# Kernel tuning notes

Measured on AMD Instinct MI355X. Metric: run time of the kernel, lower is better.

Reference implementation:

```python
import jax, jax.numpy as jnp
import numpy as np

GROUPS = 32
EPS = 1e-6

def group_norm(x, gamma, beta):
    # x: [B,C,H,W]
    B, C, H, W = x.shape
    xg = x.reshape(B, GROUPS, C // GROUPS, H, W)
    mu = xg.mean(axis=(2, 3, 4), keepdims=True)
    var = xg.var(axis=(2, 3, 4), keepdims=True)
    xn = ((xg - mu) * jax.lax.rsqrt(var + EPS)).reshape(B, C, H, W)
    return xn * gamma[None, :, None, None] + beta[None, :, None, None]

def setup_inputs() -> dict:
    key = jax.random.key(0)
    ks = jax.random.split(key, 12)
    B, C, H, W = 4, 256, 64, 64
    s = 1.0 / np.sqrt(C)
    return {
        "x": jax.random.normal(ks[0], (B, C, H, W), jnp.float32),
        "gn_gamma": jnp.ones((C,), jnp.float32),
        "gn_beta": jnp.zeros((C,), jnp.float32),
        "wq": jax.random.normal(ks[1], (C, C), jnp.float32) * s,
        "bq": jnp.zeros((C,), jnp.float32),
        "wk": jax.random.normal(ks[2], (C, C), jnp.float32) * s,
        "bk": jnp.zeros((C,), jnp.float32),
        "wv": jax.random.normal(ks[3], (C, C), jnp.float32) * s,
        "bv": jnp.zeros((C,), jnp.float32),
        "wu": jax.random.normal(ks[4], (1, C), jnp.float32) * s,
        "bu": jnp.zeros((1,), jnp.float32),
        "wp": jax.random.normal(ks[5], (C, C), jnp.float32) * s,
        "bp": jnp.zeros((C,), jnp.float32),
    }

def reference(x, gn_gamma, gn_beta, wq, bq, wk, bk, wv, bv, wu, bu, wp, bp):
    B, C, H, W = x.shape
    hw = H * W
    hn = group_norm(x, gn_gamma, gn_beta)          # norm(x); context=x so same norm
    t = hn.reshape(B, C, hw).transpose(0, 2, 1)    # [B, hw, C]
    q = t @ wq.T + bq                              # 1x1 conv == per-token linear
    k = t @ wk.T + bk
    v = t @ wv.T + bv
    u_map = jax.nn.sigmoid(t @ wu.T + bu)          # [B, hw, 1]
    scale = jnp.asarray(C, x.dtype) ** -0.5
    scores = jnp.einsum('bic,bjc->bij', q, k) * scale * u_map.transpose(0, 2, 1)
    attn = jax.nn.softmax(scores, axis=2)          # softmax over keys j
    out = jnp.einsum('bij,bjc->bic', attn, v)      # [B, hw, C]
    out = (out @ wp.T + bp).transpose(0, 2, 1).reshape(B, C, H, W)
    return (x + out, u_map)
```

## Files before the change

### kernel.cpp

```cpp
#include <hip/hip_runtime.h>
#include <cstdint>

#define B_ 4
#define C_ 256
#define HW_ 4096
#define CPG_ 8
#define M_TOT 16384
#define SCALE 0.0625f
#define FLASH_LDS 133120

typedef __attribute__((ext_vector_type(4))) float f32x4;
typedef __attribute__((ext_vector_type(16))) float f32x16;
typedef __attribute__((ext_vector_type(8))) unsigned short u16x8;
typedef __attribute__((ext_vector_type(4))) unsigned short u16x4;
typedef __attribute__((ext_vector_type(4))) unsigned int u32x4;
typedef __attribute__((ext_vector_type(8))) __bf16 bf16x8;

static __device__ __forceinline__ unsigned short f2bf(float f) {
  unsigned int u = __builtin_bit_cast(unsigned int, f);
  u += 0x7fffu + ((u >> 16) & 1u);
  return (unsigned short)(u >> 16);
}
static __device__ __forceinline__ float bf2f(unsigned short s) {
  return __builtin_bit_cast(float, ((unsigned int)s) << 16);
}
static __device__ __forceinline__ bf16x8 ldbf8(const unsigned short* p) {
  return __builtin_bit_cast(bf16x8, *(const u16x8*)p);
}
static __device__ __forceinline__ bf16x8 cvt8(const float* p) {
  f32x4 a = *(const f32x4*)p;
  f32x4 b = *(const f32x4*)(p + 4);
  u16x8 r;
  r[0] = f2bf(a[0]); r[1] = f2bf(a[1]); r[2] = f2bf(a[2]); r[3] = f2bf(a[3]);
  r[4] = f2bf(b[0]); r[5] = f2bf(b[1]); r[6] = f2bf(b[2]); r[7] = f2bf(b[3]);
  return __builtin_bit_cast(bf16x8, r);
}
static __device__ __forceinline__ void gload16(const void* g, void* l) {
  __builtin_amdgcn_global_load_lds(
      (const __attribute__((address_space(1))) unsigned int*)g,
      (__attribute__((address_space(3))) unsigned int*)l, 16, 0, 0);
}
static __device__ __forceinline__ unsigned cvtpk(float lo, float hi) {
  unsigned r;
  asm("v_cvt_pk_bf16_f32 %0, %1, %2" : "=v"(r) : "v"(lo), "v"(hi));
  return r;
}

__global__ __launch_bounds__(256) void gn_kernel(const float* __restrict__ x,
    const float* __restrict__ gamma, const float* __restrict__ beta,
    unsigned short* __restrict__ t) {
  int bg = blockIdx.x;
  int b = bg >> 5, g = bg & 31;
  const float* xp = x + ((size_t)(b * C_ + g * CPG_)) * HW_;
  float s = 0.f, ss = 0.f;
  for (int i = threadIdx.x; i < CPG_ * HW_; i += 256) {
    float v = xp[i]; s += v; ss += v * v;
  }
#pragma unroll
  for (int m = 32; m; m >>= 1) { s += __shfl_xor(s, m); ss += __shfl_xor(ss, m); }
  __shared__ float red[8];
  if ((threadIdx.x & 63) == 0) { red[threadIdx.x >> 6] = s; red[4 + (threadIdx.x >> 6)] = ss; }
  __syncthreads();
  float S = red[0] + red[1] + red[2] + red[3];
  float SS = red[4] + red[5] + red[6] + red[7];
  float mean = S * (1.f / 32768.f);
  float var = SS * (1.f / 32768.f) - mean * mean;
  float rs = rsqrtf(var + 1e-6f);
  float gam[CPG_], bet[CPG_];
#pragma unroll
  for (int cc = 0; cc < CPG_; ++cc) {
    float gm = gamma[g * CPG_ + cc];
    gam[cc] = gm * rs;
    bet[cc] = beta[g * CPG_ + cc] - mean * gm * rs;
  }
  for (int sp = threadIdx.x; sp < HW_; sp += 256) {
    u16x8 o;
#pragma unroll
    for (int cc = 0; cc < CPG_; ++cc) {
      float v = xp[cc * HW_ + sp];
      o[cc] = f2bf(v * gam[cc] + bet[cc]);
    }
    *(u16x8*)(t + ((size_t)(b * HW_ + sp)) * C_ + g * CPG_) = o;
  }
}

__global__ __launch_bounds__(256) void u_kernel(const unsigned short* __restrict__ t,
    const float* __restrict__ wu, const float* __restrict__ bu,
    float* __restrict__ uout) {
  int w = threadIdx.x >> 6, l = threadIdx.x & 63;
  int tok = blockIdx.x * 4 + w;
  u16x4 tv = *(const u16x4*)(t + (size_t)tok * C_ + l * 4);
  f32x4 wv4 = *(const f32x4*)(wu + l * 4);
  float d = bf2f(tv[0]) * wv4[0] + bf2f(tv[1]) * wv4[1] +
            bf2f(tv[2]) * wv4[2] + bf2f(tv[3]) * wv4[3];
#pragma unroll
  for (int m = 32; m; m >>= 1) d += __shfl_xor(d, m);
  if (l == 0) uout[tok] = 1.f / (1.f + __expf(-(d + bu[0])));
}

__global__ __launch_bounds__(256, 2) void qkv_kernel(const unsigned short* __restrict__ t,
    const float* __restrict__ wq, const float* __restrict__ wk, const float* __restrict__ wv,
    const float* __restrict__ bq, const float* __restrict__ bk, const float* __restrict__ bv,
    const float* __restrict__ uu,
    unsigned short* __restrict__ q, unsigned short* __restrict__ k,
    unsigned short* __restrict__ vt) {
  int mblk = blockIdx.x, nblk = blockIdx.y;
  int wsel = nblk >> 2;
  int n0 = (nblk & 3) * 64;
  const float* W = wsel == 0 ? wq : (wsel == 1 ? wk : wv);
  const float* bias = wsel == 0 ? bq : (wsel == 1 ? bk : bv);
  __shared__ unsigned short WL[64][264];
  int tid = threadIdx.x;
#pragma unroll
  for (int p = 0; p < 8; ++p) {
    int row = p * 8 + (tid >> 5);
    int kc0 = (tid & 31) * 8;
    *(bf16x8*)&WL[row][kc0] = cvt8(W + (size_t)(n0 + row) * C_ + kc0);
  }
  __syncthreads();
  int wid = tid >> 6, l = tid & 63;
  int lr = l & 15, lg = l >> 4;
  int row = mblk * 64 + wid * 16 + lr;
  f32x4 acc[4] = {};
  const unsigned short* ap = t + (size_t)row * C_ + lg * 8;
#pragma unroll
  for (int kc = 0; kc < 8; ++kc) {
    bf16x8 a = ldbf8(ap + kc * 32);
#pragma unroll
    for (int j = 0; j < 4; ++j) {
      bf16x8 bb = ldbf8(&WL[j * 16 + lr][kc * 32 + lg * 8]);
      acc[j] = __builtin_amdgcn_mfma_f32_16x16x32_bf16(a, bb, acc[j], 0, 0, 0);
    }
  }
  if (wsel < 2) {
    unsigned short* dst = wsel ? k : q;
    float su[4] = {1.f, 1.f, 1.f, 1.f};
    if (wsel == 1) {
      f32x4 u4 = *(const f32x4*)(uu + mblk * 64 + wid * 16 + lg * 4);
      su[0] = SCALE * u4[0]; su[1] = SCALE * u4[1];
      su[2] = SCALE * u4[2]; su[3] = SCALE * u4[3];
    }
#pragma unroll
    for (int j = 0; j < 4; ++j) {
      int col = n0 + j * 16 + lr;
      float bv_ = bias[col];
#pragma unroll
      for (int r = 0; r < 4; ++r)
        dst[(size_t)(mblk * 64 + wid * 16 + lg * 4 + r) * C_ + col] =
            f2bf((acc[j][r] + bv_) * su[r]);
    }
  } else {
    __shared__ float lds[64][65];
#pragma unroll
    for (int j = 0; j < 4; ++j) {
      float bv_ = bias[n0 + j * 16 + lr];
#pragma unroll
      for (int r = 0; r < 4; ++r)
        lds[wid * 16 + lg * 4 + r][j * 16 + lr] = acc[j][r] + bv_;
    }
    __syncthreads();
    int bb_ = (mblk * 64) >> 12;
    int s0 = (mblk * 64) & 4095;
    int ss = tid & 63, cc0 = tid >> 6;
    for (int cc = cc0; cc < 64; cc += 4)
      vt[((size_t)(bb_ * C_ + n0 + cc)) * HW_ + s0 + ss] = f2bf(lds[ss][cc]);
  }
}

__global__ __launch_bounds__(256, 1) void flash_kernel(const unsigned short* __restrict__ q,
    const unsigned short* __restrict__ k, const unsigned short* __restrict__ vt,
    unsigned short* __restrict__ o) {
  extern __shared__ char smem[];
  float* cmb_m = (float*)(smem + 131072);
  float* cmb_l = (float*)(smem + 131584);
  float* facw  = (float*)(smem + 132096);
  float* scrL  = (float*)(smem + 132608);

  int blk = blockIdx.x;
  int b = blk >> 6;
  int qrow0 = (blk & 63) * 64;
  int tid = threadIdx.x;
  int wid = tid >> 6, l = tid & 63;
  int l5 = l & 31, hi = l >> 5;
  int h = wid >> 1, qs = wid & 1;

  const unsigned short* kb = k + (size_t)b * HW_ * C_;
  const unsigned short* vb = vt + (size_t)b * C_ * HW_;

  bf16x8 qreg[16];
  {
    const unsigned short* qp = q + ((size_t)b * HW_ + qrow0 + qs * 32 + l5) * C_ + hi * 8;
#pragma unroll
    for (int cc = 0; cc < 16; ++cc) qreg[cc] = ldbf8(qp + cc * 16);
  }

  f32x16 oa[8];
#pragma unroll
  for (int ct = 0; ct < 8; ++ct)
#pragma unroll
    for (int r = 0; r < 16; ++r) oa[ct][r] = 0.f;
  float mrow = -1e30f, lrow = 0.f;

  int w_ = l >> 2;
  int w0_ = w_ & 1, w1_ = (w_ >> 1) & 1, w2_ = (w_ >> 2) & 1, w3_ = (w_ >> 3) & 1;
  int koffb = (l & 3) * 8;

#define STAGE(IT, BUFN)                                                          \
  {                                                                              \
    int key0n = h * 2048 + (IT) * 32;                                            \
    if (qs == 0) {                                                               \
      _Pragma("unroll")                                                          \
      for (int j = 0; j < 16; ++j) {                                             \
        int key = j * 2 + hi;                                                    \
        const unsigned short* g =                                                \
            kb + (size_t)(key0n + key) * C_ + ((l5 * 8) ^ (key * 8));            \
        gload16(g, smem + (BUFN) * 32768 + h * 16384 + j * 1024);                \
      }                                                                          \
    } else {                                                                     \
      _Pragma("unroll")                                                          \
      for (int j = 0; j < 16; ++j) {                                             \
        int j0 = j & 1;                                                          \
        int ch = (j << 4) | (w3_ << 3) | ((w2_ ^ j0) << 2) |                     \
                 ((w1_ ^ w3_) << 1) | (w0_ ^ w2_ ^ j0);                          \
        int ke = koffb ^ ((ch & 3) << 3);                                        \
        const unsigned short* g = vb + (size_t)ch * HW_ + key0n + ke;            \
        gload16(g, smem + 65536 + (BUFN) * 32768 + h * 16384 + j * 1024);        \
      }                                                                          \
    }                                                                            \
  }

  STAGE(0, 0);
  __syncthreads();

  int kx = l5 << 4;
  int vbase = (l5 * 64) ^ ((l5 >> 2) << 6);
  int ko0 = (hi * 16) ^ ((l & 3) << 4);
  int ko1 = (32 + hi * 16) ^ ((l & 3) << 4);

  for (int it = 0; it < 64; ++it) {
    int buf = it & 1;
    if (it + 1 < 64) STAGE(it + 1, buf ^ 1);

    const char* KB = smem + buf * 32768 + h * 16384;
    f32x16 s;
#pragma unroll
    for (int r = 0; r < 16; ++r) s[r] = 0.f;
#pragma unroll
    for (int cc = 0; cc < 16; ++cc) {
      bf16x8 kf = ldbf8((const unsigned short*)(KB + l5 * 512 +
                                                ((cc * 32 + hi * 16) ^ kx)));
      s = __builtin_amdgcn_mfma_f32_32x32x16_bf16(kf, qreg[cc], s, 0, 0, 0);
    }

    float mxl = s[0];
#pragma unroll
    for (int r = 1; r < 16; ++r) mxl = fmaxf(mxl, s[r]);
    float mx = fmaxf(mxl, __shfl_xor(mxl, 32));
    if (!__all(mx <= mrow + 8.f)) {
      float mnew = fmaxf(mrow, mx);
      float scr = __expf(mrow - mnew);
      mrow = mnew;
      lrow *= scr;
      if (hi == 0) scrL[wid * 32 + l5] = scr;
      float sr[16];
#pragma unroll
      for (int r = 0; r < 16; ++r)
        sr[r] = scrL[wid * 32 + (r & 3) + 8 * (r >> 2) + 4 * hi];
#pragma unroll
      for (int ct = 0; ct < 8; ++ct)
#pragma unroll
        for (int r = 0; r < 16; ++r) oa[ct][r] *= sr[r];
    }
    unsigned wp[8];
#pragma unroll
    for (int rp = 0; rp < 8; ++rp) {
      float e0 = __expf(s[2 * rp] - mrow);
      float e1 = __expf(s[2 * rp + 1] - mrow);
      lrow += e0 + e1;
      wp[rp] = cvtpk(e0, e1);
    }
    unsigned sx[8];
#pragma unroll
    for (int rp = 0; rp < 8; ++rp) sx[rp] = (unsigned)__shfl_xor((int)wp[rp], 32);
    bool hib = (hi != 0);
    u32x4 pa0u = {hib ? sx[2] : wp[0], hib ? sx[3] : wp[1],
                  hib ? wp[2] : sx[0], hib ? wp[3] : sx[1]};
    u32x4 pa1u = {hib ? sx[6] : wp[4], hib ? sx[7] : wp[5],
                  hib ? wp[6] : sx[4], hib ? wp[7] : sx[5]};
    bf16x8 pa0 = __builtin_bit_cast(bf16x8, pa0u);
    bf16x8 pa1 = __builtin_bit_cast(bf16x8, pa1u);

    const char* VB = smem + 65536 + buf * 32768 + h * 16384;
#pragma unroll
    for (int ct = 0; ct < 8; ++ct) {
      bf16x8 v0 = ldbf8((const unsigned short*)(VB + ct * 2048 + vbase + ko0));
      bf16x8 v1 = ldbf8((const unsigned short*)(VB + ct * 2048 + vbase + ko1));
      oa[ct] = __builtin_amdgcn_mfma_f32_32x32x16_bf16(pa0, v0, oa[ct], 0, 0, 0);
      oa[ct] = __builtin_amdgcn_mfma_f32_32x32x16_bf16(pa1, v1, oa[ct], 0, 0, 0);
    }
    __syncthreads();
  }
#undef STAGE

  float l_all = lrow + __shfl_xor(lrow, 32);
  if (hi == 0) { cmb_m[wid * 32 + l5] = mrow; cmb_l[wid * 32 + l5] = l_all; }
  __syncthreads();
  float mo = cmb_m[(wid ^ 2) * 32 + l5];
  float lo = cmb_l[(wid ^ 2) * 32 + l5];
  float M = fmaxf(mrow, mo);
  float el = __expf(mrow - M), eo = __expf(mo - M);
  float fac = el / (l_all * el + lo * eo);
  if (hi == 0) facw[wid * 32 + l5] = fac;
  float fr[16];
#pragma unroll
  for (int r = 0; r < 16; ++r)
    fr[r] = facw[wid * 32 + (r & 3) + 8 * (r >> 2) + 4 * hi];
  float* Ow = (float*)(smem + wid * 32768);
#pragma unroll
  for (int ct = 0; ct < 8; ++ct)
#pragma unroll
    for (int r = 0; r < 16; ++r) {
      int qr = (r & 3) + 8 * (r >> 2) + 4 * hi;
      Ow[qr * 256 + ct * 32 + l5] = oa[ct][r] * fr[r];
    }
  __syncthreads();
  for (int e = tid; e < 2048; e += 256) {
    int row = e >> 5;
    int c8 = (e & 31) * 8;
    int qs_ = row >> 5, q_ = row & 31;
    const float* p0 = (const float*)(smem + qs_ * 32768) + q_ * 256 + c8;
    const float* p1 = (const float*)(smem + (2 + qs_) * 32768) + q_ * 256 + c8;
    u16x8 ov;
#pragma unroll
    for (int j = 0; j < 8; ++j) ov[j] = f2bf(p0[j] + p1[j]);
    *(u16x8*)(o + ((size_t)b * HW_ + qrow0 + row) * C_ + c8) = ov;
  }
}

__global__ __launch_bounds__(256, 2) void proj_kernel(const unsigned short* __restrict__ o,
    const float* __restrict__ wp, const float* __restrict__ bp,
    const float* __restrict__ x, float* __restrict__ y) {
  int mblk = blockIdx.x, nblk = blockIdx.y;
  int n0 = nblk * 64;
  __shared__ unsigned short WL[64][264];
  int tid = threadIdx.x;
#pragma unroll
  for (int p = 0; p < 8; ++p) {
    int row = p * 8 + (tid >> 5);
    int kc0 = (tid & 31) * 8;
    *(bf16x8*)&WL[row][kc0] = cvt8(wp + (size_t)(n0 + row) * C_ + kc0);
  }
  __syncthreads();
  int wid = tid >> 6, l = tid & 63;
  int lr = l & 15, lg = l >> 4;
  int row = mblk * 64 + wid * 16 + lr;
  f32x4 acc[4] = {};
  const unsigned short* ap = o + (size_t)row * C_ + lg * 8;
#pragma unroll
  for (int kc = 0; kc < 8; ++kc) {
    bf16x8 a = ldbf8(ap + kc * 32);
#pragma unroll
    for (int j = 0; j < 4; ++j) {
      bf16x8 bb = ldbf8(&WL[j * 16 + lr][kc * 32 + lg * 8]);
      acc[j] = __builtin_amdgcn_mfma_f32_16x16x32_bf16(a, bb, acc[j], 0, 0, 0);
    }
  }
  __shared__ float lds[64][65];
#pragma unroll
  for (int j = 0; j < 4; ++j) {
    float bv_ = bp[n0 + j * 16 + lr];
#pragma unroll
    for (int r = 0; r < 4; ++r)
      lds[wid * 16 + lg * 4 + r][j * 16 + lr] = acc[j][r] + bv_;
  }
  __syncthreads();
  int bb_ = (mblk * 64) >> 12;
  int s0 = (mblk * 64) & 4095;
  int ss = tid & 63, cc0 = tid >> 6;
  for (int cc = cc0; cc < 64; cc += 4) {
    size_t idx = ((size_t)(bb_ * C_ + n0 + cc)) * HW_ + s0 + ss;
    y[idx] = x[idx] + lds[ss][cc];
  }
}

extern "C" void kernel_launch(void* const* d_in, const int* in_sizes, int n_in,
                              void* d_out, int out_size, void* d_ws, size_t ws_size,
                              hipStream_t stream) {
  const float* x     = (const float*)d_in[0];
  const float* gamma = (const float*)d_in[1];
  const float* beta  = (const float*)d_in[2];
  const float* wq    = (const float*)d_in[3];
  const float* bq    = (const float*)d_in[4];
  const float* wk    = (const float*)d_in[5];
  const float* bk    = (const float*)d_in[6];
  const float* wv    = (const float*)d_in[7];
  const float* bv    = (const float*)d_in[8];
  const float* wu    = (const float*)d_in[9];
  const float* bu    = (const float*)d_in[10];
  const float* wp    = (const float*)d_in[11];
  const float* bp    = (const float*)d_in[12];

  float* y = (float*)d_out;
  float* uout = y + (size_t)B_ * C_ * HW_;

  unsigned short* t  = (unsigned short*)d_ws;
  unsigned short* qb = t + (size_t)M_TOT * C_;
  unsigned short* kk = qb + (size_t)M_TOT * C_;
  unsigned short* vt = kk + (size_t)M_TOT * C_;

  hipFuncSetAttribute((const void*)flash_kernel,
                      hipFuncAttributeMaxDynamicSharedMemorySize, FLASH_LDS);

  gn_kernel<<<128, 256, 0, stream>>>(x, gamma, beta, t);
  u_kernel<<<4096, 256, 0, stream>>>(t, wu, bu, uout);
  qkv_kernel<<<dim3(256, 12), 256, 0, stream>>>(t, wq, wk, wv, bq, bk, bv, uout, qb, kk, vt);
  flash_kernel<<<256, 256, FLASH_LDS, stream>>>(qb, kk, vt, t);
  proj_kernel<<<dim3(256, 4), 256, 0, stream>>>(t, wp, bp, x, y);
}
```

Measured before the change: 228.9 us.

## Warp-specialize flash attention with dedicated loader waves and exp2-based softmax

The flash kernel grows from 256 to 512 threads. Four new producer waves only issue K/V global-to-LDS loads into the double buffer, while the original four waves only run the MFMA and softmax work, so loads can overlap compute without consuming compute-wave issue slots. The scale for K is also folded with log2(e) in qkv_kernel so the softmax can use exp2f, with the rescale threshold adjusted to match. This risks extra register pressure from launch_bounds(512,2), idle loader waves holding resources, and a barrier per iteration shared by both roles. The LDS size (133120 bytes) likely still allows only one block per CU.

```diff
diff --git a/kernel.cpp b/kernel.cpp
--- a/kernel.cpp
+++ b/kernel.cpp
@@ -7,6 +7,7 @@
 #define CPG_ 8
 #define M_TOT 16384
 #define SCALE 0.0625f
+#define LOG2E 1.44269504088896f
 #define FLASH_LDS 133120
 
 typedef __attribute__((ext_vector_type(4))) float f32x4;
@@ -137,8 +138,8 @@
     float su[4] = {1.f, 1.f, 1.f, 1.f};
     if (wsel == 1) {
       f32x4 u4 = *(const f32x4*)(uu + mblk * 64 + wid * 16 + lg * 4);
-      su[0] = SCALE * u4[0]; su[1] = SCALE * u4[1];
-      su[2] = SCALE * u4[2]; su[3] = SCALE * u4[3];
+      su[0] = SCALE * LOG2E * u4[0]; su[1] = SCALE * LOG2E * u4[1];
+      su[2] = SCALE * LOG2E * u4[2]; su[3] = SCALE * LOG2E * u4[3];
     }
 #pragma unroll
     for (int j = 0; j < 4; ++j) {
@@ -167,7 +168,7 @@
   }
 }
 
-__global__ __launch_bounds__(256, 1) void flash_kernel(const unsigned short* __restrict__ q,
+__global__ __launch_bounds__(512, 2) void flash_kernel(const unsigned short* __restrict__ q,
     const unsigned short* __restrict__ k, const unsigned short* __restrict__ vt,
     unsigned short* __restrict__ o) {
   extern __shared__ char smem[];
@@ -182,149 +183,159 @@
   int tid = threadIdx.x;
   int wid = tid >> 6, l = tid & 63;
   int l5 = l & 31, hi = l >> 5;
-  int h = wid >> 1, qs = wid & 1;
 
   const unsigned short* kb = k + (size_t)b * HW_ * C_;
   const unsigned short* vb = vt + (size_t)b * C_ * HW_;
 
-  bf16x8 qreg[16];
-  {
-    const unsigned short* qp = q + ((size_t)b * HW_ + qrow0 + qs * 32 + l5) * C_ + hi * 8;
-#pragma unroll
-    for (int cc = 0; cc < 16; ++cc) qreg[cc] = ldbf8(qp + cc * 16);
-  }
-
+  float mrow = -1e30f, lrow = 0.f;
   f32x16 oa[8];
-#pragma unroll
-  for (int ct = 0; ct < 8; ++ct)
-#pragma unroll
-    for (int r = 0; r < 16; ++r) oa[ct][r] = 0.f;
-  float mrow = -1e30f, lrow = 0.f;
-
-  int w_ = l >> 2;
-  int w0_ = w_ & 1, w1_ = (w_ >> 1) & 1, w2_ = (w_ >> 2) & 1, w3_ = (w_ >> 3) & 1;
-  int koffb = (l & 3) * 8;
-
-#define STAGE(IT, BUFN)                                                          \
-  {                                                                              \
-    int key0n = h * 2048 + (IT) * 32;                                            \
-    if (qs == 0) {                                                               \
-      _Pragma("unroll")                                                          \
-      for (int j = 0; j < 16; ++j) {                                             \
-        int key = j * 2 + hi;                                                    \
-        const unsigned short* g =                                                \
-            kb + (size_t)(key0n + key) * C_ + ((l5 * 8) ^ (key * 8));            \
-        gload16(g, smem + (BUFN) * 32768 + h * 16384 + j * 1024);                \
-      }                                                                          \
-    } else {                                                                     \
-      _Pragma("unroll")                                                          \
-      for (int j = 0; j < 16; ++j) {                                             \
-        int j0 = j & 1;                                                          \
-        int ch = (j << 4) | (w3_ << 3) | ((w2_ ^ j0) << 2) |                     \
-                 ((w1_ ^ w3_) << 1) | (w0_ ^ w2_ ^ j0);                          \
-        int ke = koffb ^ ((ch & 3) << 3);                                        \
-        const unsigned short* g = vb + (size_t)ch * HW_ + key0n + ke;            \
-        gload16(g, smem + 65536 + (BUFN) * 32768 + h * 16384 + j * 1024);        \
-      }                                                                          \
-    }                                                                            \
-  }
-
-  STAGE(0, 0);
-  __syncthreads();
-
-  int kx = l5 << 4;
-  int vbase = (l5 * 64) ^ ((l5 >> 2) << 6);
-  int ko0 = (hi * 16) ^ ((l & 3) << 4);
-  int ko1 = (32 + hi * 16) ^ ((l & 3) << 4);
-
-  for (int it = 0; it < 64; ++it) {
-    int buf = it & 1;
-    if (it + 1 < 64) STAGE(it + 1, buf ^ 1);
-
-    const char* KB = smem + buf * 32768 + h * 16384;
-    f32x16 s;
-#pragma unroll
-    for (int r = 0; r < 16; ++r) s[r] = 0.f;
-#pragma unroll
-    for (int cc = 0; cc < 16; ++cc) {
-      bf16x8 kf = ldbf8((const unsigned short*)(KB + l5 * 512 +
-                                                ((cc * 32 + hi * 16) ^ kx)));
-      s = __builtin_amdgcn_mfma_f32_32x32x16_bf16(kf, qreg[cc], s, 0, 0, 0);
-    }
-
-    float mxl = s[0];
-#pragma unroll
-    for (int r = 1; r < 16; ++r) mxl = fmaxf(mxl, s[r]);
-    float mx = fmaxf(mxl, __shfl_xor(mxl, 32));
-    if (!__all(mx <= mrow + 8.f)) {
-      float mnew = fmaxf(mrow, mx);
-      float scr = __expf(mrow - mnew);
-      mrow = mnew;
-      lrow *= scr;
-      if (hi == 0) scrL[wid * 32 + l5] = scr;
-      float sr[16];
-#pragma unroll
-      for (int r = 0; r < 16; ++r)
-        sr[r] = scrL[wid * 32 + (r & 3) + 8 * (r >> 2) + 4 * hi];
-#pragma unroll
-      for (int ct = 0; ct < 8; ++ct)
-#pragma unroll
-        for (int r = 0; r < 16; ++r) oa[ct][r] *= sr[r];
-    }
-    unsigned wp[8];
-#pragma unroll
-    for (int rp = 0; rp < 8; ++rp) {
-      float e0 = __expf(s[2 * rp] - mrow);
-      float e1 = __expf(s[2 * rp + 1] - mrow);
-      lrow += e0 + e1;
-      wp[rp] = cvtpk(e0, e1);
-    }
-    unsigned sx[8];
-#pragma unroll
-    for (int rp = 0; rp < 8; ++rp) sx[rp] = (unsigned)__shfl_xor((int)wp[rp], 32);
-    bool hib = (hi != 0);
-    u32x4 pa0u = {hib ? sx[2] : wp[0], hib ? sx[3] : wp[1],
-                  hib ? wp[2] : sx[0], hib ? wp[3] : sx[1]};
-    u32x4 pa1u = {hib ? sx[6] : wp[4], hib ? sx[7] : wp[5],
-                  hib ? wp[6] : sx[4], hib ? wp[7] : sx[5]};
-    bf16x8 pa0 = __builtin_bit_cast(bf16x8, pa0u);
-    bf16x8 pa1 = __builtin_bit_cast(bf16x8, pa1u);
-
-    const char* VB = smem + 65536 + buf * 32768 + h * 16384;
-#pragma unroll
-    for (int ct = 0; ct < 8; ++ct) {
-      bf16x8 v0 = ldbf8((const unsigned short*)(VB + ct * 2048 + vbase + ko0));
-      bf16x8 v1 = ldbf8((const unsigned short*)(VB + ct * 2048 + vbase + ko1));
-      oa[ct] = __builtin_amdgcn_mfma_f32_32x32x16_bf16(pa0, v0, oa[ct], 0, 0, 0);
-      oa[ct] = __builtin_amdgcn_mfma_f32_32x32x16_bf16(pa1, v1, oa[ct], 0, 0, 0);
-    }
+
+  if (wid >= 4) {
+    int role = wid - 4;
+    int sh = role & 1;
+    bool isK = role < 2;
+    int w_ = l >> 2;
+    int w0_ = w_ & 1, w1_ = (w_ >> 1) & 1, w2_ = (w_ >> 2) & 1, w3_ = (w_ >> 3) & 1;
+    int koffb = (l & 3) * 8;
+#define STG(IT, BUFN)                                                           \
+    {                                                                           \
+      int key0n = sh * 2048 + (IT) * 32;                                        \
+      if (isK) {                                                                \
+        _Pragma("unroll")                                                       \
+        for (int j = 0; j < 16; ++j) {                                          \
+          int key = j * 2 + hi;                                                 \
+          const unsigned short* g =                                             \
+              kb + (size_t)(key0n + key) * C_ + ((l5 * 8) ^ (key * 8));         \
+          gload16(g, smem + (BUFN) * 32768 + sh * 16384 + j * 1024);            \
+        }                                                                       \
+      } else {                                                                  \
+        _Pragma("unroll")                                                       \
+        for (int j = 0; j < 16; ++j) {                                          \
+          int j0 = j & 1;                                                       \
+          int ch = (j << 4) | (w3_ << 3) | ((w2_ ^ j0) << 2) |                  \
+                   ((w1_ ^ w3_) << 1) | (w0_ ^ w2_ ^ j0);                       \
+          int ke = koffb ^ ((ch & 3) << 3);                                     \
+          const unsigned short* g = vb + (size_t)ch * HW_ + key0n + ke;         \
+          gload16(g, smem + 65536 + (BUFN) * 32768 + sh * 16384 + j * 1024);    \
+        }                                                                       \
+      }                                                                         \
+    }
+    STG(0, 0);
     __syncthreads();
-  }
-#undef STAGE
-
-  float l_all = lrow + __shfl_xor(lrow, 32);
-  if (hi == 0) { cmb_m[wid * 32 + l5] = mrow; cmb_l[wid * 32 + l5] = l_all; }
-  __syncthreads();
-  float mo = cmb_m[(wid ^ 2) * 32 + l5];
-  float lo = cmb_l[(wid ^ 2) * 32 + l5];
-  float M = fmaxf(mrow, mo);
-  float el = __expf(mrow - M), eo = __expf(mo - M);
-  float fac = el / (l_all * el + lo * eo);
-  if (hi == 0) facw[wid * 32 + l5] = fac;
-  float fr[16];
-#pragma unroll
-  for (int r = 0; r < 16; ++r)
-    fr[r] = facw[wid * 32 + (r & 3) + 8 * (r >> 2) + 4 * hi];
-  float* Ow = (float*)(smem + wid * 32768);
-#pragma unroll
-  for (int ct = 0; ct < 8; ++ct)
-#pragma unroll
-    for (int r = 0; r < 16; ++r) {
-      int qr = (r & 3) + 8 * (r >> 2) + 4 * hi;
-      Ow[qr * 256 + ct * 32 + l5] = oa[ct][r] * fr[r];
-    }
-  __syncthreads();
-  for (int e = tid; e < 2048; e += 256) {
+    for (int it = 0; it < 64; ++it) {
+      if (it + 1 < 64) STG(it + 1, (it + 1) & 1);
+      __syncthreads();
+    }
+#undef STG
+  } else {
+    int h = wid >> 1, qs = wid & 1;
+    bf16x8 qreg[16];
+    {
+      const unsigned short* qp =
+          q + ((size_t)b * HW_ + qrow0 + qs * 32 + l5) * C_ + hi * 8;
+#pragma unroll
+      for (int cc = 0; cc < 16; ++cc) qreg[cc] = ldbf8(qp + cc * 16);
+    }
+#pragma unroll
+    for (int ct = 0; ct < 8; ++ct)
+#pragma unroll
+      for (int r = 0; r < 16; ++r) oa[ct][r] = 0.f;
+    __syncthreads();
+
+    int kx = l5 << 4;
+    int vbase = (l5 * 64) ^ ((l5 >> 2) << 6);
+    int ko0 = (hi * 16) ^ ((l & 3) << 4);
+    int ko1 = (32 + hi * 16) ^ ((l & 3) << 4);
+
+    for (int it = 0; it < 64; ++it) {
+      int buf = it & 1;
+      const char* KB = smem + buf * 32768 + h * 16384;
+      f32x16 s;
+#pragma unroll
+      for (int r = 0; r < 16; ++r) s[r] = 0.f;
+#pragma unroll
+      for (int cc = 0; cc < 16; ++cc) {
+        bf16x8 kf = ldbf8((const unsigned short*)(KB + l5 * 512 +
+                                                  ((cc * 32 + hi * 16) ^ kx)));
+        s = __builtin_amdgcn_mfma_f32_32x32x16_bf16(kf, qreg[cc], s, 0, 0, 0);
+      }
+      float mxl = s[0];
+#pragma unroll
+      for (int r = 1; r < 16; ++r) mxl = fmaxf(mxl, s[r]);
+      float mx = fmaxf(mxl, __shfl_xor(mxl, 32));
+      if (!__all(mx <= mrow + 11.f)) {
+        float mnew = fmaxf(mrow, mx);
+        float scr = exp2f(mrow - mnew);
+        mrow = mnew;
+        lrow *= scr;
+        if (hi == 0) scrL[wid * 32 + l5] = scr;
+        float sr[16];
+#pragma unroll
+        for (int r = 0; r < 16; ++r)
+          sr[r] = scrL[wid * 32 + (r & 3) + 8 * (r >> 2) + 4 * hi];
+#pragma unroll
+        for (int ct = 0; ct < 8; ++ct)
+#pragma unroll
+          for (int r = 0; r < 16; ++r) oa[ct][r] *= sr[r];
+      }
+      unsigned wp[8];
+#pragma unroll
+      for (int rp = 0; rp < 8; ++rp) {
+        float e0 = exp2f(s[2 * rp] - mrow);
+        float e1 = exp2f(s[2 * rp + 1] - mrow);
+        lrow += e0 + e1;
+        wp[rp] = cvtpk(e0, e1);
+      }
+      unsigned sx[8];
+#pragma unroll
+      for (int rp = 0; rp < 8; ++rp) sx[rp] = (unsigned)__shfl_xor((int)wp[rp], 32);
+      bool hib = (hi != 0);
+      u32x4 pa0u = {hib ? sx[2] : wp[0], hib ? sx[3] : wp[1],
+                    hib ? wp[2] : sx[0], hib ? wp[3] : sx[1]};
+      u32x4 pa1u = {hib ? sx[6] : wp[4], hib ? sx[7] : wp[5],
+                    hib ? wp[6] : sx[4], hib ? wp[7] : sx[5]};
+      bf16x8 pa0 = __builtin_bit_cast(bf16x8, pa0u);
+      bf16x8 pa1 = __builtin_bit_cast(bf16x8, pa1u);
+      const char* VB = smem + 65536 + buf * 32768 + h * 16384;
+#pragma unroll
+      for (int ct = 0; ct < 8; ++ct) {
+        bf16x8 v0 = ldbf8((const unsigned short*)(VB + ct * 2048 + vbase + ko0));
+        bf16x8 v1 = ldbf8((const unsigned short*)(VB + ct * 2048 + vbase + ko1));
+        oa[ct] = __builtin_amdgcn_mfma_f32_32x32x16_bf16(pa0, v0, oa[ct], 0, 0, 0);
+        oa[ct] = __builtin_amdgcn_mfma_f32_32x32x16_bf16(pa1, v1, oa[ct], 0, 0, 0);
+      }
+      __syncthreads();
+    }
+  }
+
+  float l_all = 0.f;
+  if (wid < 4) {
+    l_all = lrow + __shfl_xor(lrow, 32);
+    if (hi == 0) { cmb_m[wid * 32 + l5] = mrow; cmb_l[wid * 32 + l5] = l_all; }
+  }
+  __syncthreads();
+  if (wid < 4) {
+    float mo = cmb_m[(wid ^ 2) * 32 + l5];
+    float lo = cmb_l[(wid ^ 2) * 32 + l5];
+    float M = fmaxf(mrow, mo);
+    float el = exp2f(mrow - M), eo = exp2f(mo - M);
+    float fac = el / (l_all * el + lo * eo);
+    if (hi == 0) facw[wid * 32 + l5] = fac;
+    float fr[16];
+#pragma unroll
+    for (int r = 0; r < 16; ++r)
+      fr[r] = facw[wid * 32 + (r & 3) + 8 * (r >> 2) + 4 * hi];
+    float* Ow = (float*)(smem + wid * 32768);
+#pragma unroll
+    for (int ct = 0; ct < 8; ++ct)
+#pragma unroll
+      for (int r = 0; r < 16; ++r) {
+        int qr = (r & 3) + 8 * (r >> 2) + 4 * hi;
+        Ow[qr * 256 + ct * 32 + l5] = oa[ct][r] * fr[r];
+      }
+  }
+  __syncthreads();
+  for (int e = tid; e < 2048; e += 512) {
     int row = e >> 5;
     int c8 = (e & 31) * 8;
     int qs_ = row >> 5, q_ = row & 31;
@@ -414,6 +425,6 @@
   gn_kernel<<<128, 256, 0, stream>>>(x, gamma, beta, t);
   u_kernel<<<4096, 256, 0, stream>>>(t, wu, bu, uout);
   qkv_kernel<<<dim3(256, 12), 256, 0, stream>>>(t, wq, wk, wv, bq, bk, bv, uout, qb, kk, vt);
-  flash_kernel<<<256, 256, FLASH_LDS, stream>>>(qb, kk, vt, t);
+  flash_kernel<<<256, 512, FLASH_LDS, stream>>>(qb, kk, vt, t);
   proj_kernel<<<dim3(256, 4), 256, 0, stream>>>(t, wp, bp, x, y);
 }
```

Result: faster. 194.3 us (-15.1%).
